# Kernel tuning notes

Hardware: AMD Instinct MI355X
Metric: run time of the kernel (lower is better)

The kernel has to match this reference:

```python
import jax, jax.numpy as jnp
import numpy as np

N_NODES = 100000
N_EDGES = 625000
D_IN = 128
D_OUT = 128


def setup_inputs() -> dict:
    key = jax.random.key(0)
    k1, k2, k3, k4, k5 = jax.random.split(key, 5)
    feature = jax.random.normal(k1, (N_NODES, D_IN), dtype=jnp.float32)
    W = jax.random.normal(k2, (D_OUT, D_IN), dtype=jnp.float32) * (1.0 / np.sqrt(D_IN))
    b = jax.random.normal(k3, (D_OUT,), dtype=jnp.float32) * 0.01
    src = jax.random.randint(k4, (N_EDGES,), 0, N_NODES, dtype=jnp.int64)
    dst = jax.random.randint(k5, (N_EDGES,), 0, N_NODES, dtype=jnp.int64)
    return {"feature": feature, "W": W, "b": b, "src": src, "dst": dst}


def reference(feature, W, b, src, dst):
    # copy_src: gather source-node features along edges -> [E, D_IN]
    msg = feature[src]
    # mean reduce over incoming edges per destination node
    agg = jax.ops.segment_sum(msg, dst, num_segments=N_NODES)  # [N, D_IN]
    deg = jax.ops.segment_sum(jnp.ones((dst.shape[0],), feature.dtype), dst,
                              num_segments=N_NODES)  # [N]
    # DGL mean leaves nodes with zero in-degree at 0
    h = jnp.where(deg[:, None] > 0, agg / jnp.maximum(deg, 1.0)[:, None], 0.0)
    # nn.Linear: h @ W.T + b
    return h @ W.T + b
```

## Files before the change

### kernel.cpp

```cpp
#include <hip/hip_runtime.h>

#define D 128
#define CAP 32

typedef __attribute__((ext_vector_type(8))) short short8;
typedef __attribute__((ext_vector_type(4))) float f32x4;

__device__ __forceinline__ unsigned short f2bf_rne(float x) {
    unsigned int u = __float_as_uint(x);
    u += 0x7fffu + ((u >> 16) & 1u);
    return (unsigned short)(u >> 16);
}

__device__ __forceinline__ unsigned int pack_bf2(float x, float y) {
    return ((unsigned int)f2bf_rne(y) << 16) | (unsigned int)f2bf_rne(x);
}

__global__ __launch_bounds__(256)
void pack_build(const float* __restrict__ feat, const float* __restrict__ W,
                ushort* __restrict__ fb, ushort* __restrict__ Wb,
                const int* __restrict__ src, const int* __restrict__ dst,
                int* __restrict__ cnt, int* __restrict__ bucket,
                int n4, int n_edges, int edgeBlocks) {
    int bx = blockIdx.x;
    if (bx < edgeBlocks) {
        int e = bx * 256 + threadIdx.x;
        if (e < n_edges) {
            int d = dst[e];
            int p = atomicAdd(cnt + d, 1);
            if (p < CAP) bucket[(size_t)d * CAP + p] = src[e];
        }
        return;
    }
    int i = (bx - edgeBlocks) * 256 + threadIdx.x;
    if (i < n4) {
        float4 v = ((const float4*)feat)[i];
        ushort4 o;
        o.x = f2bf_rne(v.x); o.y = f2bf_rne(v.y);
        o.z = f2bf_rne(v.z); o.w = f2bf_rne(v.w);
        ((ushort4*)fb)[i] = o;
    } else if (i < n4 + 32) {
        ((ushort4*)fb)[i] = make_ushort4(0, 0, 0, 0);
    } else if (i < n4 + 32 + 4096) {
        int j = i - (n4 + 32);
        float4 v = ((const float4*)W)[j];
        ushort4 o;
        o.x = f2bf_rne(v.x); o.y = f2bf_rne(v.y);
        o.z = f2bf_rne(v.z); o.w = f2bf_rne(v.w);
        ((ushort4*)Wb)[j] = o;
    }
}

__global__ __launch_bounds__(256, 4)
void agg_gemm(const ushort* __restrict__ fb,
              const int* __restrict__ cnt,
              const int* __restrict__ bucket,
              const ushort* __restrict__ Wb,
              const float* __restrict__ b,
              float* __restrict__ out,
              int n_nodes) {
    __shared__ ushort hs[32 * 136];
    int t = threadIdx.x;
    int lane = t & 63;
    int wave = t >> 6;
    int nb = blockIdx.x * 32;
    int base = nb + wave * 8;

    int g = lane >> 4;
    int s = lane & 15;
    int g16 = lane & 48;

    int myc = (lane < 8) ? cnt[base + lane] : 0;

    const int* bkt = bucket + (size_t)base * CAP;
    int idsA0 = bkt[g * 32 + s];
    int idsA1 = bkt[g * 32 + 16 + s];
    int idsB0 = bkt[128 + g * 32 + s];
    int idsB1 = bkt[128 + g * 32 + 16 + s];

    int dA = __shfl(myc, g);
    int dB = __shfl(myc, 4 + g);
    int cA = min(dA, CAP), cB = min(dB, CAP);
    idsA0 = (s < cA)      ? idsA0 : n_nodes;
    idsA1 = (16 + s < cA) ? idsA1 : n_nodes;
    idsB0 = (s < cB)      ? idsB0 : n_nodes;
    idsB1 = (16 + s < cB) ? idsB1 : n_nodes;

    int mm = cA > cB ? cA : cB;
    mm = max(mm, __shfl_xor(mm, 16));
    mm = max(mm, __shfl_xor(mm, 32));
    int mmax = mm;

    float fA[8], fB[8];
#pragma unroll
    for (int i = 0; i < 8; ++i) { fA[i] = 0.0f; fB[i] = 0.0f; }

    const char* fbb = (const char*)fb;
    unsigned int colb = (unsigned int)s * 16u;

#define GATH1(dst, ids0_, ids1_, jj) { \
    int idr_ = ((jj) < 16) ? (ids0_) : (ids1_); \
    unsigned int rr_ = ((jj) < mmax) ? (unsigned int)__shfl(idr_, g16 + ((jj) & 15)) \
                                     : (unsigned int)n_nodes; \
    dst = *(const uint4*)(fbb + ((rr_ << 8) + colb)); }

#define ACC8(v, f) { \
    f[0] += __uint_as_float((v).x << 16); f[1] += __uint_as_float((v).x & 0xffff0000u); \
    f[2] += __uint_as_float((v).y << 16); f[3] += __uint_as_float((v).y & 0xffff0000u); \
    f[4] += __uint_as_float((v).z << 16); f[5] += __uint_as_float((v).z & 0xffff0000u); \
    f[6] += __uint_as_float((v).w << 16); f[7] += __uint_as_float((v).w & 0xffff0000u); }

    uint4 a0, b0, a1, b1, a2, b2, a3, b3;
    GATH1(a0, idsA0, idsA1, 0); GATH1(b0, idsB0, idsB1, 0);
    GATH1(a1, idsA0, idsA1, 1); GATH1(b1, idsB0, idsB1, 1);
    for (int j = 0; j < mmax; j += 4) {
        GATH1(a2, idsA0, idsA1, j + 2); GATH1(b2, idsB0, idsB1, j + 2);
        GATH1(a3, idsA0, idsA1, j + 3); GATH1(b3, idsB0, idsB1, j + 3);
        ACC8(a0, fA); ACC8(b0, fB);
        ACC8(a1, fA); ACC8(b1, fB);
        GATH1(a0, idsA0, idsA1, j + 4); GATH1(b0, idsB0, idsB1, j + 4);
        GATH1(a1, idsA0, idsA1, j + 5); GATH1(b1, idsB0, idsB1, j + 5);
        ACC8(a2, fA); ACC8(b2, fB);
        ACC8(a3, fA); ACC8(b3, fB);
    }
#undef GATH1
#undef ACC8

    float invA = dA > 0 ? 1.0f / (float)dA : 0.0f;
    float invB = dB > 0 ? 1.0f / (float)dB : 0.0f;

    unsigned int* hsu = (unsigned int*)hs;
    int rA = wave * 8 + g;
    int rB = wave * 8 + 4 + g;
    *(uint4*)&hsu[rA * 68 + s * 4] = make_uint4(
        pack_bf2(fA[0] * invA, fA[1] * invA), pack_bf2(fA[2] * invA, fA[3] * invA),
        pack_bf2(fA[4] * invA, fA[5] * invA), pack_bf2(fA[6] * invA, fA[7] * invA));
    *(uint4*)&hsu[rB * 68 + s * 4] = make_uint4(
        pack_bf2(fB[0] * invB, fB[1] * invB), pack_bf2(fB[2] * invB, fB[3] * invB),
        pack_bf2(fB[4] * invB, fB[5] * invB), pack_bf2(fB[6] * invB, fB[7] * invB));
    __syncthreads();

    int mt = wave & 1;
    int nh = wave >> 1;
    int lane16 = lane & 15;
    int lq = lane >> 4;

    f32x4 acc[4] = {{0,0,0,0},{0,0,0,0},{0,0,0,0},{0,0,0,0}};
#pragma unroll
    for (int ks = 0; ks < 4; ++ks) {
        short8 afrg = *(const short8*)&hs[(mt * 16 + lane16) * 136 + ks * 32 + lq * 8];
#pragma unroll
        for (int tt = 0; tt < 4; ++tt) {
            short8 bfrg = *(const short8*)&Wb[(size_t)(nh * 64 + tt * 16 + lane16) * D + ks * 32 + lq * 8];
            acc[tt] = __builtin_amdgcn_mfma_f32_16x16x32_bf16(afrg, bfrg, acc[tt], 0, 0, 0);
        }
    }

#pragma unroll
    for (int tt = 0; tt < 4; ++tt) {
        int o = nh * 64 + tt * 16 + lane16;
        float bb = b[o];
        int node = nb + mt * 16 + lq * 4;
#pragma unroll
        for (int r = 0; r < 4; ++r) {
            out[(size_t)(node + r) * D + o] = acc[tt][r] + bb;
        }
    }
}

extern "C" void kernel_launch(void* const* d_in, const int* in_sizes, int n_in,
                              void* d_out, int out_size, void* d_ws, size_t ws_size,
                              hipStream_t stream) {
    const float* feat = (const float*)d_in[0];
    const float* W    = (const float*)d_in[1];
    const float* bia  = (const float*)d_in[2];
    const int* src = (const int*)d_in[3];
    const int* dst = (const int*)d_in[4];
    float* out = (float*)d_out;

    int n_nodes = in_sizes[0] / D;
    int n_edges = in_sizes[3];

    size_t off = 0;
    auto alloc = [&](size_t bytes) { size_t p = off; off = (off + bytes + 4095) & ~(size_t)4095; return p; };
    size_t cnt_off    = alloc((size_t)n_nodes * sizeof(int));
    size_t bucket_off = alloc((size_t)n_nodes * CAP * sizeof(int));
    size_t wb_off     = alloc((size_t)D * D * sizeof(ushort));
    size_t fb_off     = alloc((size_t)(n_nodes + 1) * D * sizeof(ushort));

    int*    cnt    = (int*)((char*)d_ws + cnt_off);
    int*    bucket = (int*)((char*)d_ws + bucket_off);
    ushort* Wb     = (ushort*)((char*)d_ws + wb_off);
    ushort* fb     = (ushort*)((char*)d_ws + fb_off);

    int n4 = n_nodes * (D / 4);
    int G  = n4 + 32 + (D * D / 4);

    int edgeBlocks = (n_edges + 255) / 256;
    int packBlocks = (G + 255) / 256;

    hipMemsetAsync(cnt, 0, (size_t)n_nodes * sizeof(int), stream);
    pack_build<<<edgeBlocks + packBlocks, 256, 0, stream>>>(feat, W, fb, Wb, src, dst,
                                                            cnt, bucket, n4, n_edges, edgeBlocks);
    agg_gemm<<<n_nodes / 32, 256, 0, stream>>>(fb, cnt, bucket, Wb, bia, out, n_nodes);
}
```

Before: 180.2 us.

## Gather fp32 features directly instead of pre-packing a bf16 feature copy

Drops the pre-pass that converted the whole feature matrix to bf16 in a workspace buffer. The aggregation kernel now gathers fp32 rows straight from the input and masks padded edges with a multiply-by-zero FMA instead of pointing them at a zero sentinel row. This removes a full read and write pass over the feature table, but each gather now moves twice as many bytes (512 B rows instead of 256 B). It also keeps aggregation in full fp32 precision.

New measurement: 189.9 us. +5.4%, slower.

```diff
diff --git a/kernel.cpp b/kernel.cpp
--- a/kernel.cpp
+++ b/kernel.cpp
@@ -17,11 +17,10 @@
 }
 
 __global__ __launch_bounds__(256)
-void pack_build(const float* __restrict__ feat, const float* __restrict__ W,
-                ushort* __restrict__ fb, ushort* __restrict__ Wb,
-                const int* __restrict__ src, const int* __restrict__ dst,
-                int* __restrict__ cnt, int* __restrict__ bucket,
-                int n4, int n_edges, int edgeBlocks) {
+void build_w(const float* __restrict__ W, ushort* __restrict__ Wb,
+             const int* __restrict__ src, const int* __restrict__ dst,
+             int* __restrict__ cnt, int* __restrict__ bucket,
+             int n_edges, int edgeBlocks) {
     int bx = blockIdx.x;
     if (bx < edgeBlocks) {
         int e = bx * 256 + threadIdx.x;
@@ -32,17 +31,8 @@
         }
         return;
     }
-    int i = (bx - edgeBlocks) * 256 + threadIdx.x;
-    if (i < n4) {
-        float4 v = ((const float4*)feat)[i];
-        ushort4 o;
-        o.x = f2bf_rne(v.x); o.y = f2bf_rne(v.y);
-        o.z = f2bf_rne(v.z); o.w = f2bf_rne(v.w);
-        ((ushort4*)fb)[i] = o;
-    } else if (i < n4 + 32) {
-        ((ushort4*)fb)[i] = make_ushort4(0, 0, 0, 0);
-    } else if (i < n4 + 32 + 4096) {
-        int j = i - (n4 + 32);
+    int j = (bx - edgeBlocks) * 256 + threadIdx.x;
+    if (j < D * D / 4) {
         float4 v = ((const float4*)W)[j];
         ushort4 o;
         o.x = f2bf_rne(v.x); o.y = f2bf_rne(v.y);
@@ -52,7 +42,7 @@
 }
 
 __global__ __launch_bounds__(256, 4)
-void agg_gemm(const ushort* __restrict__ fb,
+void agg_gemm(const float* __restrict__ feat,
               const int* __restrict__ cnt,
               const int* __restrict__ bucket,
               const ushort* __restrict__ Wb,
@@ -81,10 +71,10 @@
     int dA = __shfl(myc, g);
     int dB = __shfl(myc, 4 + g);
     int cA = min(dA, CAP), cB = min(dB, CAP);
-    idsA0 = (s < cA)      ? idsA0 : n_nodes;
-    idsA1 = (16 + s < cA) ? idsA1 : n_nodes;
-    idsB0 = (s < cB)      ? idsB0 : n_nodes;
-    idsB1 = (16 + s < cB) ? idsB1 : n_nodes;
+    idsA0 = (s < cA)      ? idsA0 : 0;
+    idsA1 = (16 + s < cA) ? idsA1 : 0;
+    idsB0 = (s < cB)      ? idsB0 : 0;
+    idsB1 = (16 + s < cB) ? idsB1 : 0;
 
     int mm = cA > cB ? cA : cB;
     mm = max(mm, __shfl_xor(mm, 16));
@@ -95,36 +85,42 @@
 #pragma unroll
     for (int i = 0; i < 8; ++i) { fA[i] = 0.0f; fB[i] = 0.0f; }
 
-    const char* fbb = (const char*)fb;
-    unsigned int colb = (unsigned int)s * 16u;
+    const char* fbb = (const char*)feat;
+    unsigned int colb = (unsigned int)s * 32u;
 
-#define GATH1(dst, ids0_, ids1_, jj) { \
+#define GATH(dL, dH, ids0_, ids1_, jj) { \
     int idr_ = ((jj) < 16) ? (ids0_) : (ids1_); \
-    unsigned int rr_ = ((jj) < mmax) ? (unsigned int)__shfl(idr_, g16 + ((jj) & 15)) \
-                                     : (unsigned int)n_nodes; \
-    dst = *(const uint4*)(fbb + ((rr_ << 8) + colb)); }
+    unsigned int rr_ = ((jj) < mmax) ? (unsigned int)__shfl(idr_, g16 + ((jj) & 15)) : 0u; \
+    const char* p_ = fbb + ((rr_ << 9) + colb); \
+    dL = *(const float4*)p_; \
+    dH = *(const float4*)(p_ + 16); }
 
-#define ACC8(v, f) { \
-    f[0] += __uint_as_float((v).x << 16); f[1] += __uint_as_float((v).x & 0xffff0000u); \
-    f[2] += __uint_as_float((v).y << 16); f[3] += __uint_as_float((v).y & 0xffff0000u); \
-    f[4] += __uint_as_float((v).z << 16); f[5] += __uint_as_float((v).z & 0xffff0000u); \
-    f[6] += __uint_as_float((v).w << 16); f[7] += __uint_as_float((v).w & 0xffff0000u); }
+#define ACCF(vL, vH, f, vm) { \
+    f[0] = fmaf(vm, (vL).x, f[0]); f[1] = fmaf(vm, (vL).y, f[1]); \
+    f[2] = fmaf(vm, (vL).z, f[2]); f[3] = fmaf(vm, (vL).w, f[3]); \
+    f[4] = fmaf(vm, (vH).x, f[4]); f[5] = fmaf(vm, (vH).y, f[5]); \
+    f[6] = fmaf(vm, (vH).z, f[6]); f[7] = fmaf(vm, (vH).w, f[7]); }
 
-    uint4 a0, b0, a1, b1, a2, b2, a3, b3;
-    GATH1(a0, idsA0, idsA1, 0); GATH1(b0, idsB0, idsB1, 0);
-    GATH1(a1, idsA0, idsA1, 1); GATH1(b1, idsB0, idsB1, 1);
+    float4 aL0, aH0, aL1, aH1, aL2, aH2, aL3, aH3;
+    float4 bL0, bH0, bL1, bH1, bL2, bH2, bL3, bH3;
+    GATH(aL0, aH0, idsA0, idsA1, 0); GATH(bL0, bH0, idsB0, idsB1, 0);
+    GATH(aL1, aH1, idsA0, idsA1, 1); GATH(bL1, bH1, idsB0, idsB1, 1);
     for (int j = 0; j < mmax; j += 4) {
-        GATH1(a2, idsA0, idsA1, j + 2); GATH1(b2, idsB0, idsB1, j + 2);
-        GATH1(a3, idsA0, idsA1, j + 3); GATH1(b3, idsB0, idsB1, j + 3);
-        ACC8(a0, fA); ACC8(b0, fB);
-        ACC8(a1, fA); ACC8(b1, fB);
-        GATH1(a0, idsA0, idsA1, j + 4); GATH1(b0, idsB0, idsB1, j + 4);
-        GATH1(a1, idsA0, idsA1, j + 5); GATH1(b1, idsB0, idsB1, j + 5);
-        ACC8(a2, fA); ACC8(b2, fB);
-        ACC8(a3, fA); ACC8(b3, fB);
+        GATH(aL2, aH2, idsA0, idsA1, j + 2); GATH(bL2, bH2, idsB0, idsB1, j + 2);
+        GATH(aL3, aH3, idsA0, idsA1, j + 3); GATH(bL3, bH3, idsB0, idsB1, j + 3);
+        ACCF(aL0, aH0, fA, (j     < cA) ? 1.0f : 0.0f);
+        ACCF(bL0, bH0, fB, (j     < cB) ? 1.0f : 0.0f);
+        ACCF(aL1, aH1, fA, (j + 1 < cA) ? 1.0f : 0.0f);
+        ACCF(bL1, bH1, fB, (j + 1 < cB) ? 1.0f : 0.0f);
+        GATH(aL0, aH0, idsA0, idsA1, j + 4); GATH(bL0, bH0, idsB0, idsB1, j + 4);
+        GATH(aL1, aH1, idsA0, idsA1, j + 5); GATH(bL1, bH1, idsB0, idsB1, j + 5);
+        ACCF(aL2, aH2, fA, (j + 2 < cA) ? 1.0f : 0.0f);
+        ACCF(bL2, bH2, fB, (j + 2 < cB) ? 1.0f : 0.0f);
+        ACCF(aL3, aH3, fA, (j + 3 < cA) ? 1.0f : 0.0f);
+        ACCF(bL3, bH3, fB, (j + 3 < cB) ? 1.0f : 0.0f);
     }
-#undef GATH1
-#undef ACC8
+#undef GATH
+#undef ACCF
 
     float invA = dA > 0 ? 1.0f / (float)dA : 0.0f;
     float invB = dB > 0 ? 1.0f / (float)dB : 0.0f;
@@ -186,21 +182,16 @@
     size_t cnt_off    = alloc((size_t)n_nodes * sizeof(int));
     size_t bucket_off = alloc((size_t)n_nodes * CAP * sizeof(int));
     size_t wb_off     = alloc((size_t)D * D * sizeof(ushort));
-    size_t fb_off     = alloc((size_t)(n_nodes + 1) * D * sizeof(ushort));
 
     int*    cnt    = (int*)((char*)d_ws + cnt_off);
     int*    bucket = (int*)((char*)d_ws + bucket_off);
     ushort* Wb     = (ushort*)((char*)d_ws + wb_off);
-    ushort* fb     = (ushort*)((char*)d_ws + fb_off);
-
-    int n4 = n_nodes * (D / 4);
-    int G  = n4 + 32 + (D * D / 4);
 
     int edgeBlocks = (n_edges + 255) / 256;
-    int packBlocks = (G + 255) / 256;
+    int wBlocks    = (D * D / 4 + 255) / 256;
 
     hipMemsetAsync(cnt, 0, (size_t)n_nodes * sizeof(int), stream);
-    pack_build<<<edgeBlocks + packBlocks, 256, 0, stream>>>(feat, W, fb, Wb, src, dst,
-                                                            cnt, bucket, n4, n_edges, edgeBlocks);
-    agg_gemm<<<n_nodes / 32, 256, 0, stream>>>(fb, cnt, bucket, Wb, bia, out, n_nodes);
+    build_w<<<edgeBlocks + wBlocks, 256, 0, stream>>>(W, Wb, src, dst,
+                                                      cnt, bucket, n_edges, edgeBlocks);
+    agg_gemm<<<n_nodes / 32, 256, 0, stream>>>(feat, cnt, bucket, Wb, bia, out, n_nodes);
 }
```

## Stage neighbor feature gathers through LDS with async global_load_lds double buffering

Applied to the files above, without the earlier changes.

Replaces the register-based software-pipelined gather of bf16 neighbor rows with direct global-to-LDS async loads into a per-wave double-buffered staging area, synchronized with explicit vmcnt waits. The intent is to keep more gather loads in flight and free vector registers, hiding memory latency of the irregular row fetches. It adds 64 KB of LDS per block, which cuts occupancy, and drops the occupancy hint from launch_bounds. It also adds an extra LDS read per element.

After: 190.2 us. 1.06x slower.

```diff
diff --git a/kernel.cpp b/kernel.cpp
--- a/kernel.cpp
+++ b/kernel.cpp
@@ -51,7 +51,18 @@
     }
 }
 
-__global__ __launch_bounds__(256, 4)
+__device__ __forceinline__ void gl_lds16(const void* g, void* l) {
+    __builtin_amdgcn_global_load_lds(
+        (const __attribute__((address_space(1))) unsigned int*)g,
+        (__attribute__((address_space(3))) unsigned int*)l,
+        16, 0, 0);
+}
+
+#define VMCNT(n) { \
+    asm volatile("s_waitcnt vmcnt(" #n ")" ::: "memory"); \
+    __builtin_amdgcn_sched_barrier(0); }
+
+__global__ __launch_bounds__(256)
 void agg_gemm(const ushort* __restrict__ fb,
               const int* __restrict__ cnt,
               const int* __restrict__ bucket,
@@ -60,6 +71,7 @@
               float* __restrict__ out,
               int n_nodes) {
     __shared__ ushort hs[32 * 136];
+    __shared__ char stage[4][2][8192];
     int t = threadIdx.x;
     int lane = t & 63;
     int wave = t >> 6;
@@ -69,6 +81,7 @@
     int g = lane >> 4;
     int s = lane & 15;
     int g16 = lane & 48;
+    int s16 = s * 16;
 
     int myc = (lane < 8) ? cnt[base + lane] : 0;
 
@@ -96,13 +109,24 @@
     for (int i = 0; i < 8; ++i) { fA[i] = 0.0f; fB[i] = 0.0f; }
 
     const char* fbb = (const char*)fb;
-    unsigned int colb = (unsigned int)s * 16u;
-
-#define GATH1(dst, ids0_, ids1_, jj) { \
-    int idr_ = ((jj) < 16) ? (ids0_) : (ids1_); \
-    unsigned int rr_ = ((jj) < mmax) ? (unsigned int)__shfl(idr_, g16 + ((jj) & 15)) \
-                                     : (unsigned int)n_nodes; \
-    dst = *(const uint4*)(fbb + ((rr_ << 8) + colb)); }
+    unsigned int zr = (unsigned int)n_nodes;
+    char* stg = &stage[wave][0][0];
+
+    auto issue = [&](int c) {
+        char* lb = stg + ((c & 1) << 13);
+#pragma unroll
+        for (int q = 0; q < 4; ++q) {
+            int jj = c * 4 + q;
+            int srcl = g16 + (jj & 15);
+            int ia = (jj < 16) ? idsA0 : idsA1;
+            int ib = (jj < 16) ? idsB0 : idsB1;
+            unsigned int ra = (jj < mmax) ? (unsigned int)__shfl(ia, srcl) : zr;
+            unsigned int rb = (jj < mmax) ? (unsigned int)__shfl(ib, srcl) : zr;
+            gl_lds16(fbb + (((size_t)ra) << 8) + s16, lb + q * 2048);
+            gl_lds16(fbb + (((size_t)rb) << 8) + s16, lb + q * 2048 + 1024);
+        }
+        __builtin_amdgcn_sched_barrier(0);
+    };
 
 #define ACC8(v, f) { \
     f[0] += __uint_as_float((v).x << 16); f[1] += __uint_as_float((v).x & 0xffff0000u); \
@@ -110,20 +134,28 @@
     f[4] += __uint_as_float((v).z << 16); f[5] += __uint_as_float((v).z & 0xffff0000u); \
     f[6] += __uint_as_float((v).w << 16); f[7] += __uint_as_float((v).w & 0xffff0000u); }
 
-    uint4 a0, b0, a1, b1, a2, b2, a3, b3;
-    GATH1(a0, idsA0, idsA1, 0); GATH1(b0, idsB0, idsB1, 0);
-    GATH1(a1, idsA0, idsA1, 1); GATH1(b1, idsB0, idsB1, 1);
-    for (int j = 0; j < mmax; j += 4) {
-        GATH1(a2, idsA0, idsA1, j + 2); GATH1(b2, idsB0, idsB1, j + 2);
-        GATH1(a3, idsA0, idsA1, j + 3); GATH1(b3, idsB0, idsB1, j + 3);
-        ACC8(a0, fA); ACC8(b0, fB);
-        ACC8(a1, fA); ACC8(b1, fB);
-        GATH1(a0, idsA0, idsA1, j + 4); GATH1(b0, idsB0, idsB1, j + 4);
-        GATH1(a1, idsA0, idsA1, j + 5); GATH1(b1, idsB0, idsB1, j + 5);
-        ACC8(a2, fA); ACC8(b2, fB);
-        ACC8(a3, fA); ACC8(b3, fB);
-    }
-#undef GATH1
+    auto readback = [&](int c) {
+        const char* rb_ = stg + ((c & 1) << 13);
+#pragma unroll
+        for (int q = 0; q < 4; ++q) {
+            uint4 va = *(const uint4*)(rb_ + q * 2048 +        g * 256 + s16);
+            uint4 vb = *(const uint4*)(rb_ + q * 2048 + 1024 + g * 256 + s16);
+            ACC8(va, fA); ACC8(vb, fB);
+        }
+        __builtin_amdgcn_sched_barrier(0);
+    };
+
+    int nch = (mmax + 3) >> 2;
+    if (nch > 0) {
+        issue(0);
+        for (int c = 0; c < nch - 1; ++c) {
+            issue(c + 1);
+            VMCNT(8);
+            readback(c);
+        }
+        VMCNT(0);
+        readback(nch - 1);
+    }
 #undef ACC8
 
     float invA = dA > 0 ? 1.0f / (float)dA : 0.0f;
```
